# Kernel tuning notes

Hardware: AMD Instinct MI355X
Metric: run time of the kernel (lower is better)

The kernel has to match this reference:

```python
import jax, jax.numpy as jnp
import numpy as np

MARGIN = 0.3
EPS = 1e-12

def setup_inputs() -> dict:
    key = jax.random.key(0)
    k1, k2 = jax.random.split(key)
    B, D, NUM_IDS = 1024, 2048, 256
    features = jax.random.normal(k1, (B, D), dtype=jnp.float32)
    labels = jax.random.randint(k2, (B,), 0, NUM_IDS, dtype=jnp.int64)
    return {"features": features, "labels": labels}

def _pairwise_euclidean(features):
    # dist^2 = |x_i|^2 + |x_j|^2 - 2 x_i . x_j, clamped then sqrt (as in torch ref)
    sq = jnp.sum(features * features, axis=1)  # [B]
    d2 = sq[:, None] + sq[None, :] - 2.0 * (features @ features.T)
    return jnp.sqrt(jnp.maximum(d2, EPS))

def reference(features, labels):
    B = features.shape[0]
    dist = _pairwise_euclidean(features)  # [B, B]
    eq = labels[None, :] == labels[:, None]  # [B, B]; eq[i] == labels_equal row i
    eye = jnp.eye(B, dtype=bool)
    pos_mask = eq & ~eye
    neg_mask = ~eq
    neg_inf = jnp.float32(-jnp.inf)
    pos_inf = jnp.float32(jnp.inf)
    hardest_pos = jnp.max(jnp.where(pos_mask, dist, neg_inf), axis=1)  # [B]
    hardest_neg = jnp.min(jnp.where(neg_mask, dist, pos_inf), axis=1)  # [B]
    valid = jnp.any(pos_mask, axis=1) & jnp.any(neg_mask, axis=1)  # rows contributing a triplet
    per_row = jax.nn.relu(hardest_pos - hardest_neg + MARGIN)
    per_row = jnp.where(valid, per_row, 0.0)
    n_valid = jnp.sum(valid)
    loss = jnp.sum(per_row) / jnp.maximum(n_valid, 1).astype(per_row.dtype)
    num_active = jnp.sum(valid & (per_row > 0))
    return loss, num_active
```

## Files before the change

### kernel.cpp

```cpp
#include <hip/hip_runtime.h>
#include <math.h>

#define B_SZ 1024
#define D_SZ 2048
#define MARGIN 0.3f

typedef _Float16 f16x8 __attribute__((ext_vector_type(8)));
typedef float f32x16 __attribute__((ext_vector_type(16)));

union FragU { uint4 u; f16x8 v; };
union H4 { _Float16 h[4]; uint2 u; };



__global__ __launch_bounds__(256) void prep_kernel(const float* __restrict__ F,
                                                   _Float16* __restrict__ Fh,
                                                   float* __restrict__ sqpart,
                                                   int* __restrict__ hp,
                                                   int* __restrict__ hn,
                                                   int* __restrict__ flags) {
    __shared__ _Float16 slab[64][136];
    __shared__ float part[64];

    const int b = blockIdx.x;
    const int i = b >> 4;
    const int kseg = b & 15;
    const int t = threadIdx.x;
    const int lane = t & 63;
    const int w = t >> 6;

    const int idx = b * 256 + t;
    if (idx < 1024) {
        hp[idx] = 0;
        hn[idx] = 0x7F800000;
        flags[idx] = 0;
    }

#pragma unroll
    for (int q = 0; q < 8; ++q) {
        const int rl = q * 8 + (t >> 5);
        const int c4 = (t & 31) * 4;
        const float4 v = *(const float4*)(F + (size_t)(i * 64 + rl) * D_SZ +
                                          kseg * 128 + c4);
        float s = v.x * v.x + v.y * v.y + v.z * v.z + v.w * v.w;
#pragma unroll
        for (int mask = 1; mask < 32; mask <<= 1) s += __shfl_xor(s, mask);
        if ((t & 31) == 0) part[rl] = s;
        H4 p;
        p.h[0] = (_Float16)v.x; p.h[1] = (_Float16)v.y;
        p.h[2] = (_Float16)v.z; p.h[3] = (_Float16)v.w;
        *(uint2*)&slab[rl][c4] = p.u;
    }
    __syncthreads();

    if (t < 64) sqpart[kseg * 1024 + i * 64 + t] = part[t];

#pragma unroll
    for (int q2 = 0; q2 < 4; ++q2) {
        const int u = w * 4 + q2;
        const int kb = u >> 1;
        const int rg = u & 1;
        const uint4 d = *(const uint4*)&slab[rg * 32 + (lane & 31)]
                                          [kb * 16 + (lane >> 5) * 8];
        const size_t g = (size_t)((i * 128 + kseg * 8 + kb) * 2 + rg);
        *(uint4*)((char*)Fh + g * 1024 + (size_t)lane * 16) = d;
    }
}


__global__ __launch_bounds__(256) void dist_f16_kernel(
    const _Float16* __restrict__ Fh, const int* __restrict__ labels,
    const float* __restrict__ sqpart, int* __restrict__ hp,
    int* __restrict__ hn, int* __restrict__ flags) {
    __shared__ __align__(16) char comb[65536];
    __shared__ int labR[64], labC[64];
    __shared__ float sqR[64], sqC[64];

    const int t = threadIdx.x;
    const int lane = t & 63;
    const int w = t >> 6;

    const int tileId = (blockIdx.x & 7) * 32 + (blockIdx.x >> 3);
    const int bi = tileId >> 4;
    const int bj = tileId & 15;
    const int rowBase = bi * 64, colBase = bj * 64;

    if (t < 128) {
        const int e = t & 63;
        const int side = t >> 6;
        const int row = (side ? colBase : rowBase) + e;
        float s = 0.f;
#pragma unroll
        for (int p = 0; p < 16; ++p) s += sqpart[p * 1024 + row];
        if (side) { sqC[e] = s; labC[e] = labels[row]; }
        else      { sqR[e] = s; labR[e] = labels[row]; }
    }
    __syncthreads();

    const char* __restrict__ FhB = (const char*)Fh;

    f32x16 acc[2][2];
#pragma unroll
    for (int a = 0; a < 2; ++a)
#pragma unroll
        for (int c = 0; c < 2; ++c)
#pragma unroll
            for (int e = 0; e < 16; ++e) acc[a][c][e] = 0.f;

    uint4 A[3][4], Bv[3][4];

#define LOADAB(s, buf)                                                          \
    {                                                                           \
        const int kb16 = w * 32 + (s) * 2;                                      \
        _Pragma("unroll")                                                       \
        for (int kl = 0; kl < 2; ++kl)                                          \
            _Pragma("unroll")                                                   \
            for (int rg = 0; rg < 2; ++rg) {                                    \
                A[buf][kl * 2 + rg] = *(const uint4*)(FhB +                     \
                    (size_t)(((bi * 128 + kb16 + kl) * 2 + rg)) * 1024 +        \
                    (size_t)lane * 16);                                         \
                Bv[buf][kl * 2 + rg] = *(const uint4*)(FhB +                    \
                    (size_t)(((bj * 128 + kb16 + kl) * 2 + rg)) * 1024 +        \
                    (size_t)lane * 16);                                         \
            }                                                                   \
    }

#define MFMA8(buf)                                                              \
    {                                                                           \
        _Pragma("unroll")                                                       \
        for (int kl = 0; kl < 2; ++kl) {                                        \
            FragU a0, a1, v0, v1;                                               \
            a0.u = A[buf][kl * 2 + 0];                                          \
            a1.u = A[buf][kl * 2 + 1];                                          \
            v0.u = Bv[buf][kl * 2 + 0];                                         \
            v1.u = Bv[buf][kl * 2 + 1];                                         \
            acc[0][0] = __builtin_amdgcn_mfma_f32_32x32x16_f16(a0.v, v0.v, acc[0][0], 0, 0, 0); \
            acc[0][1] = __builtin_amdgcn_mfma_f32_32x32x16_f16(a0.v, v1.v, acc[0][1], 0, 0, 0); \
            acc[1][0] = __builtin_amdgcn_mfma_f32_32x32x16_f16(a1.v, v0.v, acc[1][0], 0, 0, 0); \
            acc[1][1] = __builtin_amdgcn_mfma_f32_32x32x16_f16(a1.v, v1.v, acc[1][1], 0, 0, 0); \
        }                                                                       \
    }

    LOADAB(0, 0);
    LOADAB(1, 1);
    LOADAB(2, 2);
#pragma unroll
    for (int s = 0; s < 16; ++s) {
        const int c = s % 3;
        MFMA8(c);
        if (s + 3 < 16) LOADAB(s + 3, c);
    }

#pragma unroll
    for (int fr = 0; fr < 2; ++fr)
#pragma unroll
        for (int fc = 0; fc < 2; ++fc)
#pragma unroll
            for (int g = 0; g < 4; ++g) {
                float4 v;
                v.x = acc[fr][fc][g * 4 + 0];
                v.y = acc[fr][fc][g * 4 + 1];
                v.z = acc[fr][fc][g * 4 + 2];
                v.w = acc[fr][fc][g * 4 + 3];
                *(float4*)(comb + ((size_t)((w * 16 + (fr * 2 + fc) * 4 + g) * 64 + lane)) * 16) = v;
            }
    __syncthreads();

    const int fr = w >> 1, fc = w & 1;
    float cS[16];
#pragma unroll
    for (int e = 0; e < 16; ++e) cS[e] = 0.f;
#pragma unroll
    for (int wp = 0; wp < 4; ++wp)
#pragma unroll
        for (int g = 0; g < 4; ++g) {
            float4 v = *(const float4*)(comb + ((size_t)((wp * 16 + w * 4 + g) * 64 + lane)) * 16);
            cS[g * 4 + 0] += v.x;
            cS[g * 4 + 1] += v.y;
            cS[g * 4 + 2] += v.z;
            cS[g * 4 + 3] += v.w;
        }

    const float BIG = 1e38f;
    const int h = lane >> 5;
    const int colL = fc * 32 + (lane & 31);
    const int j = colBase + colL;
    const int lj = labC[colL];
    const float sqj = sqC[colL];
#pragma unroll
    for (int k = 0; k < 16; ++k) {
        const int rowL = fr * 32 + (k & 3) + 8 * (k >> 2) + 4 * h;
        const int i = rowBase + rowL;
        const float d2 = sqR[rowL] + sqj - 2.f * cS[k];
        const float d = sqrtf(fmaxf(d2, 1e-12f));
        const bool eq = (labR[rowL] == lj);
        const bool isPos = eq && (i != j);
        float pv = isPos ? d : -BIG;
        float nv = eq ? BIG : d;
        int pf = (isPos ? 1 : 0) | (eq ? 0 : 2);
#pragma unroll
        for (int mask = 1; mask < 32; mask <<= 1) {
            pv = fmaxf(pv, __shfl_xor(pv, mask));
            nv = fminf(nv, __shfl_xor(nv, mask));
            pf |= __shfl_xor(pf, mask);
        }
        if ((lane & 31) == 0) {
            if (pf & 1) atomicMax(&hp[i], __float_as_int(pv));
            if (pf & 2) atomicMin(&hn[i], __float_as_int(nv));
            if (pf) atomicOr(&flags[i], pf);
        }
    }
#undef LOADAB
#undef MFMA8
}


__global__ __launch_bounds__(1024) void final_kernel(const int* __restrict__ hp,
                                                     const int* __restrict__ hn,
                                                     const int* __restrict__ flags,
                                                     float* __restrict__ out) {
    __shared__ float ssum[16];
    __shared__ int svalid[16], sact[16];
    const int t = threadIdx.x;
    const float hpv = __int_as_float(hp[t]);
    const float hnv = __int_as_float(hn[t]);
    const int f = flags[t];
    const bool valid = (f == 3);
    float pr = fmaxf(hpv - hnv + MARGIN, 0.f);
    if (!valid) pr = 0.f;
    int act = (valid && pr > 0.f) ? 1 : 0;
    int vld = valid ? 1 : 0;
    float s = pr;
    for (int off = 32; off; off >>= 1) {
        s += __shfl_down(s, off);
        act += __shfl_down(act, off);
        vld += __shfl_down(vld, off);
    }
    if ((t & 63) == 0) {
        ssum[t >> 6] = s;
        svalid[t >> 6] = vld;
        sact[t >> 6] = act;
    }
    __syncthreads();
    if (t == 0) {
        float tot = 0.f;
        int nv = 0, na = 0;
#pragma unroll
        for (int i = 0; i < 16; ++i) {
            tot += ssum[i];
            nv += svalid[i];
            na += sact[i];
        }
        out[0] = tot / (float)(nv > 1 ? nv : 1);
        out[1] = (float)na;
    }
}


#define BM 64
#define BN 64
#define BK 32

__global__ __launch_bounds__(256) void sq_kernel(const float* __restrict__ F,
                                                 float* __restrict__ sq) {
    int row = blockIdx.x;
    const float4* r4 = (const float4*)(F + (size_t)row * D_SZ);
    int t = threadIdx.x;
    float s = 0.f;
#pragma unroll
    for (int q = 0; q < 2; ++q) {
        float4 v = r4[t + q * 256];
        s += v.x * v.x + v.y * v.y + v.z * v.z + v.w * v.w;
    }
    for (int off = 32; off; off >>= 1) s += __shfl_down(s, off);
    __shared__ float wsum[4];
    if ((t & 63) == 0) wsum[t >> 6] = s;
    __syncthreads();
    if (t == 0) sq[row] = wsum[0] + wsum[1] + wsum[2] + wsum[3];
}

__global__ __launch_bounds__(256) void init_kernel(int* __restrict__ hp,
                                                   int* __restrict__ hn,
                                                   int* __restrict__ flags) {
    int i = blockIdx.x * 256 + threadIdx.x;
    hp[i] = 0;
    hn[i] = 0x7F800000;
    flags[i] = 0;
}

__global__ __launch_bounds__(256) void dist_f32_kernel(
    const float* __restrict__ F, const int* __restrict__ labels,
    const float* __restrict__ sq, int* __restrict__ hp, int* __restrict__ hn,
    int* __restrict__ flags) {
    __shared__ float As[BK][BM];
    __shared__ float Bs[BK][BN];
    __shared__ int labR[BM], labC[BN];
    __shared__ float sqR[BM], sqC[BN];

    const int rowBase = blockIdx.y * BM;
    const int colBase = blockIdx.x * BN;
    const int t = threadIdx.x;
    const int tx = t & 15;
    const int ty = t >> 4;

    if (t < 64) {
        labR[t] = labels[rowBase + t];
        sqR[t] = sq[rowBase + t];
    } else if (t < 128) {
        int u = t - 64;
        labC[u] = labels[colBase + u];
        sqC[u] = sq[colBase + u];
    }

    float acc[4][4] = {{0.f}};
    const int m = t & 63;
    const int q = t >> 6;
    const float* aRow = F + (size_t)(rowBase + m) * D_SZ + q * 8;
    const float* bRow = F + (size_t)(colBase + m) * D_SZ + q * 8;

    for (int k0 = 0; k0 < D_SZ; k0 += BK) {
        float4 a0 = *(const float4*)(aRow + k0);
        float4 a1 = *(const float4*)(aRow + k0 + 4);
        float4 b0 = *(const float4*)(bRow + k0);
        float4 b1 = *(const float4*)(bRow + k0 + 4);
        __syncthreads();
        int kb = q * 8;
        As[kb + 0][m] = a0.x; As[kb + 1][m] = a0.y;
        As[kb + 2][m] = a0.z; As[kb + 3][m] = a0.w;
        As[kb + 4][m] = a1.x; As[kb + 5][m] = a1.y;
        As[kb + 6][m] = a1.z; As[kb + 7][m] = a1.w;
        Bs[kb + 0][m] = b0.x; Bs[kb + 1][m] = b0.y;
        Bs[kb + 2][m] = b0.z; Bs[kb + 3][m] = b0.w;
        Bs[kb + 4][m] = b1.x; Bs[kb + 5][m] = b1.y;
        Bs[kb + 6][m] = b1.z; Bs[kb + 7][m] = b1.w;
        __syncthreads();
#pragma unroll
        for (int kk = 0; kk < BK; ++kk) {
            float4 a = *(const float4*)&As[kk][ty * 4];
            float4 b = *(const float4*)&Bs[kk][tx * 4];
            acc[0][0] += a.x * b.x; acc[0][1] += a.x * b.y;
            acc[0][2] += a.x * b.z; acc[0][3] += a.x * b.w;
            acc[1][0] += a.y * b.x; acc[1][1] += a.y * b.y;
            acc[1][2] += a.y * b.z; acc[1][3] += a.y * b.w;
            acc[2][0] += a.z * b.x; acc[2][1] += a.z * b.y;
            acc[2][2] += a.z * b.z; acc[2][3] += a.z * b.w;
            acc[3][0] += a.w * b.x; acc[3][1] += a.w * b.y;
            acc[3][2] += a.w * b.z; acc[3][3] += a.w * b.w;
        }
    }

    float mp[4], mn[4];
    int pf[4];
#pragma unroll
    for (int rr = 0; rr < 4; ++rr) {
        const int i = rowBase + ty * 4 + rr;
        const int li = labR[ty * 4 + rr];
        const float si = sqR[ty * 4 + rr];
        mp[rr] = -3.4e38f;
        mn[rr] = 3.4e38f;
        pf[rr] = 0;
#pragma unroll
        for (int c = 0; c < 4; ++c) {
            const int j = colBase + tx * 4 + c;
            const float d2 = si + sqC[tx * 4 + c] - 2.f * acc[rr][c];
            const float dist = sqrtf(fmaxf(d2, 1e-12f));
            const bool eq = (li == labC[tx * 4 + c]);
            if (eq && (i != j)) {
                mp[rr] = fmaxf(mp[rr], dist);
                pf[rr] |= 1;
            }
            if (!eq) {
                mn[rr] = fminf(mn[rr], dist);
                pf[rr] |= 2;
            }
        }
    }
#pragma unroll
    for (int mask = 1; mask < 16; mask <<= 1)
#pragma unroll
        for (int rr = 0; rr < 4; ++rr) {
            mp[rr] = fmaxf(mp[rr], __shfl_xor(mp[rr], mask));
            mn[rr] = fminf(mn[rr], __shfl_xor(mn[rr], mask));
            pf[rr] |= __shfl_xor(pf[rr], mask);
        }
    if (tx == 0) {
#pragma unroll
        for (int rr = 0; rr < 4; ++rr) {
            const int i = rowBase + ty * 4 + rr;
            if (pf[rr] & 1) atomicMax(&hp[i], __float_as_int(mp[rr]));
            if (pf[rr] & 2) atomicMin(&hn[i], __float_as_int(mn[rr]));
            if (pf[rr]) atomicOr(&flags[i], pf[rr]);
        }
    }
}


extern "C" void kernel_launch(void* const* d_in, const int* in_sizes, int n_in,
                              void* d_out, int out_size, void* d_ws, size_t ws_size,
                              hipStream_t stream) {
    const float* F = (const float*)d_in[0];
    const int* labels = (const int*)d_in[1];
    float* out = (float*)d_out;
    char* ws = (char*)d_ws;

    const size_t FH = (size_t)B_SZ * D_SZ * 2;
    const size_t SQP = 16 * 1024 * sizeof(float);
    const size_t need = FH + SQP + 12 * 1024;

    if (ws_size >= need) {
        _Float16* Fh = (_Float16*)ws;
        float* sqpart = (float*)(ws + FH);
        char* tail = ws + FH + SQP;
        int* hp = (int*)tail;
        int* hn = (int*)(tail + 4096);
        int* flags = (int*)(tail + 8192);

        prep_kernel<<<256, 256, 0, stream>>>(F, Fh, sqpart, hp, hn, flags);
        dist_f16_kernel<<<256, 256, 0, stream>>>(Fh, labels, sqpart, hp, hn, flags);
        final_kernel<<<1, 1024, 0, stream>>>(hp, hn, flags, out);
    } else {
        float* sq = (float*)ws;
        int* hp = (int*)(ws + 4096);
        int* hn = (int*)(ws + 8192);
        int* flags = (int*)(ws + 12288);

        sq_kernel<<<B_SZ, 256, 0, stream>>>(F, sq);
        init_kernel<<<B_SZ / 256, 256, 0, stream>>>(hp, hn, flags);
        dim3 grid(B_SZ / BN, B_SZ / BM);
        dist_f32_kernel<<<grid, 256, 0, stream>>>(F, labels, sq, hp, hn, flags);
        final_kernel<<<1, 1024, 0, stream>>>(hp, hn, flags, out);
    }
}
```

Before: 37.63 us.

## Split K across eight waves per block with two-stage cross-wave reduction

The distance tile kernel now launches 512 threads per block, giving each of eight waves half as many K steps. Partial accumulators are combined in two stages: the upper four waves add into the lower four through LDS, then the lower four exchange sub-tile fragments for the final sum. The prefetch pipeline now keeps four buffers, and the tile-to-XCD mapping is changed so each XCD covers a contiguous 4x8 block of tiles, meant to improve L2 reuse. The goal is more latency hiding per CU, paid for with an extra barrier, more LDS traffic and possible register pressure under the 512,2 launch bound.

```diff
diff --git a/kernel.cpp b/kernel.cpp
--- a/kernel.cpp
+++ b/kernel.cpp
@@ -68,7 +68,7 @@
 }
 
 
-__global__ __launch_bounds__(256) void dist_f16_kernel(
+__global__ __launch_bounds__(512, 2) void dist_f16_kernel(
     const _Float16* __restrict__ Fh, const int* __restrict__ labels,
     const float* __restrict__ sqpart, int* __restrict__ hp,
     int* __restrict__ hn, int* __restrict__ flags) {
@@ -80,9 +80,10 @@
     const int lane = t & 63;
     const int w = t >> 6;
 
-    const int tileId = (blockIdx.x & 7) * 32 + (blockIdx.x >> 3);
-    const int bi = tileId >> 4;
-    const int bj = tileId & 15;
+    const int xcd = blockIdx.x & 7;
+    const int cidx = blockIdx.x >> 3;
+    const int bi = (xcd >> 1) * 4 + (cidx >> 3);
+    const int bj = (xcd & 1) * 8 + (cidx & 7);
     const int rowBase = bi * 64, colBase = bj * 64;
 
     if (t < 128) {
@@ -107,11 +108,11 @@
 #pragma unroll
             for (int e = 0; e < 16; ++e) acc[a][c][e] = 0.f;
 
-    uint4 A[3][4], Bv[3][4];
+    uint4 A[4][4], Bv[4][4];
 
 #define LOADAB(s, buf)                                                          \
     {                                                                           \
-        const int kb16 = w * 32 + (s) * 2;                                      \
+        const int kb16 = w * 16 + (s) * 2;                                      \
         _Pragma("unroll")                                                       \
         for (int kl = 0; kl < 2; ++kl)                                          \
             _Pragma("unroll")                                                   \
@@ -145,16 +146,52 @@
     LOADAB(1, 1);
     LOADAB(2, 2);
 #pragma unroll
-    for (int s = 0; s < 16; ++s) {
-        const int c = s % 3;
-        MFMA8(c);
-        if (s + 3 < 16) LOADAB(s + 3, c);
-    }
-
-#pragma unroll
-    for (int fr = 0; fr < 2; ++fr)
-#pragma unroll
-        for (int fc = 0; fc < 2; ++fc)
+    for (int s = 0; s < 8; ++s) {
+        if (s + 3 < 8) LOADAB(s + 3, (s + 3) & 3);
+        MFMA8(s & 3);
+    }
+#undef LOADAB
+#undef MFMA8
+
+    if (w >= 4) {
+        char* r = comb + (w - 4) * 16384;
+#pragma unroll
+        for (int fr = 0; fr < 2; ++fr)
+#pragma unroll
+            for (int fc = 0; fc < 2; ++fc)
+#pragma unroll
+                for (int g = 0; g < 4; ++g) {
+                    float4 v;
+                    v.x = acc[fr][fc][g * 4 + 0];
+                    v.y = acc[fr][fc][g * 4 + 1];
+                    v.z = acc[fr][fc][g * 4 + 2];
+                    v.w = acc[fr][fc][g * 4 + 3];
+                    *(float4*)(r + (size_t)(((fr * 2 + fc) * 4 + g) * 64 + lane) * 16) = v;
+                }
+    }
+    __syncthreads();
+    if (w < 4) {
+        const char* r = comb + w * 16384;
+#pragma unroll
+        for (int fr = 0; fr < 2; ++fr)
+#pragma unroll
+            for (int fc = 0; fc < 2; ++fc)
+#pragma unroll
+                for (int g = 0; g < 4; ++g) {
+                    float4 v = *(const float4*)(r + (size_t)(((fr * 2 + fc) * 4 + g) * 64 + lane) * 16);
+                    acc[fr][fc][g * 4 + 0] += v.x;
+                    acc[fr][fc][g * 4 + 1] += v.y;
+                    acc[fr][fc][g * 4 + 2] += v.z;
+                    acc[fr][fc][g * 4 + 3] += v.w;
+                }
+    }
+    __syncthreads();
+    if (w < 4) {
+#pragma unroll
+        for (int f = 0; f < 4; ++f) {
+            if (f == w) continue;
+            char* r = comb + (size_t)(f * 4 + w) * 4096;
+            const int fr = f >> 1, fc = f & 1;
 #pragma unroll
             for (int g = 0; g < 4; ++g) {
                 float4 v;
@@ -162,56 +199,60 @@
                 v.y = acc[fr][fc][g * 4 + 1];
                 v.z = acc[fr][fc][g * 4 + 2];
                 v.w = acc[fr][fc][g * 4 + 3];
-                *(float4*)(comb + ((size_t)((w * 16 + (fr * 2 + fc) * 4 + g) * 64 + lane)) * 16) = v;
-            }
-    __syncthreads();
-
-    const int fr = w >> 1, fc = w & 1;
-    float cS[16];
-#pragma unroll
-    for (int e = 0; e < 16; ++e) cS[e] = 0.f;
-#pragma unroll
-    for (int wp = 0; wp < 4; ++wp)
-#pragma unroll
-        for (int g = 0; g < 4; ++g) {
-            float4 v = *(const float4*)(comb + ((size_t)((wp * 16 + w * 4 + g) * 64 + lane)) * 16);
-            cS[g * 4 + 0] += v.x;
-            cS[g * 4 + 1] += v.y;
-            cS[g * 4 + 2] += v.z;
-            cS[g * 4 + 3] += v.w;
-        }
-
-    const float BIG = 1e38f;
-    const int h = lane >> 5;
-    const int colL = fc * 32 + (lane & 31);
-    const int j = colBase + colL;
-    const int lj = labC[colL];
-    const float sqj = sqC[colL];
-#pragma unroll
-    for (int k = 0; k < 16; ++k) {
-        const int rowL = fr * 32 + (k & 3) + 8 * (k >> 2) + 4 * h;
-        const int i = rowBase + rowL;
-        const float d2 = sqR[rowL] + sqj - 2.f * cS[k];
-        const float d = sqrtf(fmaxf(d2, 1e-12f));
-        const bool eq = (labR[rowL] == lj);
-        const bool isPos = eq && (i != j);
-        float pv = isPos ? d : -BIG;
-        float nv = eq ? BIG : d;
-        int pf = (isPos ? 1 : 0) | (eq ? 0 : 2);
-#pragma unroll
-        for (int mask = 1; mask < 32; mask <<= 1) {
-            pv = fmaxf(pv, __shfl_xor(pv, mask));
-            nv = fminf(nv, __shfl_xor(nv, mask));
-            pf |= __shfl_xor(pf, mask);
-        }
-        if ((lane & 31) == 0) {
-            if (pf & 1) atomicMax(&hp[i], __float_as_int(pv));
-            if (pf & 2) atomicMin(&hn[i], __float_as_int(nv));
-            if (pf) atomicOr(&flags[i], pf);
-        }
-    }
-#undef LOADAB
-#undef MFMA8
+                *(float4*)(r + (size_t)(g * 64 + lane) * 16) = v;
+            }
+        }
+    }
+    __syncthreads();
+    if (w < 4) {
+        const int fr = w >> 1, fc = w & 1;
+        float cS[16];
+#pragma unroll
+        for (int e = 0; e < 16; ++e) cS[e] = acc[fr][fc][e];
+#pragma unroll
+        for (int u = 0; u < 4; ++u) {
+            if (u == w) continue;
+            const char* r = comb + (size_t)(w * 4 + u) * 4096;
+#pragma unroll
+            for (int g = 0; g < 4; ++g) {
+                float4 v = *(const float4*)(r + (size_t)(g * 64 + lane) * 16);
+                cS[g * 4 + 0] += v.x;
+                cS[g * 4 + 1] += v.y;
+                cS[g * 4 + 2] += v.z;
+                cS[g * 4 + 3] += v.w;
+            }
+        }
+
+        const float BIG = 1e38f;
+        const int h = lane >> 5;
+        const int colL = fc * 32 + (lane & 31);
+        const int j = colBase + colL;
+        const int lj = labC[colL];
+        const float sqj = sqC[colL];
+#pragma unroll
+        for (int k = 0; k < 16; ++k) {
+            const int rowL = fr * 32 + (k & 3) + 8 * (k >> 2) + 4 * h;
+            const int i = rowBase + rowL;
+            const float d2 = sqR[rowL] + sqj - 2.f * cS[k];
+            const float d = sqrtf(fmaxf(d2, 1e-12f));
+            const bool eq = (labR[rowL] == lj);
+            const bool isPos = eq && (i != j);
+            float pv = isPos ? d : -BIG;
+            float nv = eq ? BIG : d;
+            int pf = (isPos ? 1 : 0) | (eq ? 0 : 2);
+#pragma unroll
+            for (int mask = 1; mask < 32; mask <<= 1) {
+                pv = fmaxf(pv, __shfl_xor(pv, mask));
+                nv = fminf(nv, __shfl_xor(nv, mask));
+                pf |= __shfl_xor(pf, mask);
+            }
+            if ((lane & 31) == 0) {
+                if (pf & 1) atomicMax(&hp[i], __float_as_int(pv));
+                if (pf & 2) atomicMin(&hn[i], __float_as_int(nv));
+                if (pf) atomicOr(&flags[i], pf);
+            }
+        }
+    }
 }
 
 
@@ -416,7 +457,7 @@
         int* flags = (int*)(tail + 8192);
 
         prep_kernel<<<256, 256, 0, stream>>>(F, Fh, sqpart, hp, hn, flags);
-        dist_f16_kernel<<<256, 256, 0, stream>>>(Fh, labels, sqpart, hp, hn, flags);
+        dist_f16_kernel<<<256, 512, 0, stream>>>(Fh, labels, sqpart, hp, hn, flags);
         final_kernel<<<1, 1024, 0, stream>>>(hp, hn, flags, out);
     } else {
         float* sq = (float*)ws;
```

New measurement: 42.60 us. +13.2%, slower.

## Stage GEMM operands through LDS via direct global-to-LDS async loads

Applied to the files above, without the earlier changes.

Replaces register-buffered global loads in the distance GEMM with global_load_lds transfers into a per-wave triple-buffered LDS stage, using explicit vmcnt waits to overlap loads with MFMA. Operands are then read back from LDS for the MFMAs. The aim is to free VGPRs and make prefetch more asynchronous. In exchange it adds an LDS round trip, grows shared memory to 96KB (limiting occupancy), and depends on hand-tuned vmcnt counts being correct.

```diff
diff --git a/kernel.cpp b/kernel.cpp
--- a/kernel.cpp
+++ b/kernel.cpp
@@ -10,6 +10,9 @@
 
 union FragU { uint4 u; f16x8 v; };
 union H4 { _Float16 h[4]; uint2 u; };
+
+#define AS1 __attribute__((address_space(1)))
+#define AS3 __attribute__((address_space(3)))
 
 
 
@@ -68,11 +71,13 @@
 }
 
 
+#define WAVE_STAGE (3 * 8192)
+
 __global__ __launch_bounds__(256) void dist_f16_kernel(
     const _Float16* __restrict__ Fh, const int* __restrict__ labels,
     const float* __restrict__ sqpart, int* __restrict__ hp,
     int* __restrict__ hn, int* __restrict__ flags) {
-    __shared__ __align__(16) char comb[65536];
+    __shared__ __align__(16) char stage[4 * WAVE_STAGE];
     __shared__ int labR[64], labC[64];
     __shared__ float sqR[64], sqC[64];
 
@@ -96,8 +101,11 @@
         else      { sqR[e] = s; labR[e] = labels[row]; }
     }
     __syncthreads();
+    asm volatile("s_waitcnt vmcnt(0)" ::: "memory");
 
     const char* __restrict__ FhB = (const char*)Fh;
+    char* wbase = stage + w * WAVE_STAGE;
+    const char* rbase = wbase + lane * 16;
 
     f32x16 acc[2][2];
 #pragma unroll
@@ -107,50 +115,61 @@
 #pragma unroll
             for (int e = 0; e < 16; ++e) acc[a][c][e] = 0.f;
 
-    uint4 A[3][4], Bv[3][4];
-
-#define LOADAB(s, buf)                                                          \
-    {                                                                           \
-        const int kb16 = w * 32 + (s) * 2;                                      \
-        _Pragma("unroll")                                                       \
-        for (int kl = 0; kl < 2; ++kl)                                          \
-            _Pragma("unroll")                                                   \
-            for (int rg = 0; rg < 2; ++rg) {                                    \
-                A[buf][kl * 2 + rg] = *(const uint4*)(FhB +                     \
-                    (size_t)(((bi * 128 + kb16 + kl) * 2 + rg)) * 1024 +        \
-                    (size_t)lane * 16);                                         \
-                Bv[buf][kl * 2 + rg] = *(const uint4*)(FhB +                    \
-                    (size_t)(((bj * 128 + kb16 + kl) * 2 + rg)) * 1024 +        \
-                    (size_t)lane * 16);                                         \
-            }                                                                   \
-    }
-
-#define MFMA8(buf)                                                              \
-    {                                                                           \
-        _Pragma("unroll")                                                       \
-        for (int kl = 0; kl < 2; ++kl) {                                        \
-            FragU a0, a1, v0, v1;                                               \
-            a0.u = A[buf][kl * 2 + 0];                                          \
-            a1.u = A[buf][kl * 2 + 1];                                          \
-            v0.u = Bv[buf][kl * 2 + 0];                                         \
-            v1.u = Bv[buf][kl * 2 + 1];                                         \
-            acc[0][0] = __builtin_amdgcn_mfma_f32_32x32x16_f16(a0.v, v0.v, acc[0][0], 0, 0, 0); \
-            acc[0][1] = __builtin_amdgcn_mfma_f32_32x32x16_f16(a0.v, v1.v, acc[0][1], 0, 0, 0); \
-            acc[1][0] = __builtin_amdgcn_mfma_f32_32x32x16_f16(a1.v, v0.v, acc[1][0], 0, 0, 0); \
-            acc[1][1] = __builtin_amdgcn_mfma_f32_32x32x16_f16(a1.v, v1.v, acc[1][1], 0, 0, 0); \
-        }                                                                       \
-    }
-
-    LOADAB(0, 0);
-    LOADAB(1, 1);
-    LOADAB(2, 2);
-#pragma unroll
-    for (int s = 0; s < 16; ++s) {
-        const int c = s % 3;
-        MFMA8(c);
-        if (s + 3 < 16) LOADAB(s + 3, c);
-    }
-
+    auto ISSUE = [&](int s, int b) {
+        const int kb16 = w * 32 + s * 2;
+        const size_t aOff = (size_t)((bi * 128 + kb16) * 2) * 1024 + (size_t)lane * 16;
+        const size_t bOff = (size_t)((bj * 128 + kb16) * 2) * 1024 + (size_t)lane * 16;
+        char* dA = wbase + b * 8192;
+#pragma unroll
+        for (int c = 0; c < 4; ++c)
+            __builtin_amdgcn_global_load_lds(
+                (const AS1 void*)(FhB + aOff + c * 1024),
+                (AS3 void*)(dA + c * 1024), 16, 0, 0);
+#pragma unroll
+        for (int c = 0; c < 4; ++c)
+            __builtin_amdgcn_global_load_lds(
+                (const AS1 void*)(FhB + bOff + c * 1024),
+                (AS3 void*)(dA + 4096 + c * 1024), 16, 0, 0);
+    };
+    auto COMPUTE = [&](int b) {
+        const char* rb = rbase + b * 8192;
+#pragma unroll
+        for (int kl = 0; kl < 2; ++kl) {
+            FragU a0, a1, v0, v1;
+            a0.u = *(const uint4*)(rb + (kl * 2 + 0) * 1024);
+            a1.u = *(const uint4*)(rb + (kl * 2 + 1) * 1024);
+            v0.u = *(const uint4*)(rb + 4096 + (kl * 2 + 0) * 1024);
+            v1.u = *(const uint4*)(rb + 4096 + (kl * 2 + 1) * 1024);
+            acc[0][0] = __builtin_amdgcn_mfma_f32_32x32x16_f16(a0.v, v0.v, acc[0][0], 0, 0, 0);
+            acc[0][1] = __builtin_amdgcn_mfma_f32_32x32x16_f16(a0.v, v1.v, acc[0][1], 0, 0, 0);
+            acc[1][0] = __builtin_amdgcn_mfma_f32_32x32x16_f16(a1.v, v0.v, acc[1][0], 0, 0, 0);
+            acc[1][1] = __builtin_amdgcn_mfma_f32_32x32x16_f16(a1.v, v1.v, acc[1][1], 0, 0, 0);
+        }
+    };
+
+#define WAIT16 asm volatile("s_waitcnt vmcnt(16)" ::: "memory"); __builtin_amdgcn_sched_barrier(0)
+#define WAIT8  asm volatile("s_waitcnt vmcnt(8)"  ::: "memory"); __builtin_amdgcn_sched_barrier(0)
+#define WAIT0  asm volatile("s_waitcnt vmcnt(0)"  ::: "memory"); __builtin_amdgcn_sched_barrier(0)
+
+    ISSUE(0, 0);
+    ISSUE(1, 1);
+    for (int s3 = 0; s3 < 12; s3 += 3) {
+        ISSUE(s3 + 2, 2); WAIT16; COMPUTE(0);
+        ISSUE(s3 + 3, 0); WAIT16; COMPUTE(1);
+        ISSUE(s3 + 4, 1); WAIT16; COMPUTE(2);
+    }
+    ISSUE(14, 2); WAIT16; COMPUTE(0);
+    ISSUE(15, 0); WAIT16; COMPUTE(1);
+    WAIT8;  COMPUTE(2);
+    WAIT0;  COMPUTE(0);
+
+#undef WAIT16
+#undef WAIT8
+#undef WAIT0
+
+    __syncthreads();
+
+    char* cb = stage;
 #pragma unroll
     for (int fr = 0; fr < 2; ++fr)
 #pragma unroll
@@ -162,7 +181,7 @@
                 v.y = acc[fr][fc][g * 4 + 1];
                 v.z = acc[fr][fc][g * 4 + 2];
                 v.w = acc[fr][fc][g * 4 + 3];
-                *(float4*)(comb + ((size_t)((w * 16 + (fr * 2 + fc) * 4 + g) * 64 + lane)) * 16) = v;
+                *(float4*)(cb + ((size_t)((w * 16 + (fr * 2 + fc) * 4 + g) * 64 + lane)) * 16) = v;
             }
     __syncthreads();
 
@@ -174,7 +193,7 @@
     for (int wp = 0; wp < 4; ++wp)
 #pragma unroll
         for (int g = 0; g < 4; ++g) {
-            float4 v = *(const float4*)(comb + ((size_t)((wp * 16 + w * 4 + g) * 64 + lane)) * 16);
+            float4 v = *(const float4*)(cb + ((size_t)((wp * 16 + w * 4 + g) * 64 + lane)) * 16);
             cS[g * 4 + 0] += v.x;
             cS[g * 4 + 1] += v.y;
             cS[g * 4 + 2] += v.z;
@@ -210,8 +229,6 @@
             if (pf) atomicOr(&flags[i], pf);
         }
     }
-#undef LOADAB
-#undef MFMA8
 }
 
 
```

Result: faster. 31.97 us (median of 2 runs) (-15.0%).

## Split K across eight waves with tree reduction in dist kernel

Applied to the files above, without the earlier changes.

Doubles the dist kernel's block to 512 threads so eight waves each handle one eighth of the K dimension, with a shallower two-deep register double-buffer instead of the three-deep prefetch. Partial accumulators are combined through a three-stage shared-memory tree reduction, and wave 0 alone then runs the distance/mask epilogue for the whole 64x64 tile. The aim is more latency hiding per CU from more waves and fewer registers per wave. The cost is extra barriers and a serialized epilogue on a single wave.

```diff
diff --git a/kernel.cpp b/kernel.cpp
--- a/kernel.cpp
+++ b/kernel.cpp
@@ -68,11 +68,11 @@
 }
 
 
-__global__ __launch_bounds__(256) void dist_f16_kernel(
+__global__ __launch_bounds__(512) void dist_f16_kernel(
     const _Float16* __restrict__ Fh, const int* __restrict__ labels,
     const float* __restrict__ sqpart, int* __restrict__ hp,
     int* __restrict__ hn, int* __restrict__ flags) {
-    __shared__ __align__(16) char comb[65536];
+    __shared__ __align__(16) char cb[65536];
     __shared__ int labR[64], labC[64];
     __shared__ float sqR[64], sqC[64];
 
@@ -98,6 +98,8 @@
     __syncthreads();
 
     const char* __restrict__ FhB = (const char*)Fh;
+    const char* pA0 = FhB + (size_t)((bi * 128 + w * 16) * 2) * 1024 + (size_t)lane * 16;
+    const char* pB0 = FhB + (size_t)((bj * 128 + w * 16) * 2) * 1024 + (size_t)lane * 16;
 
     f32x16 acc[2][2];
 #pragma unroll
@@ -107,111 +109,120 @@
 #pragma unroll
             for (int e = 0; e < 16; ++e) acc[a][c][e] = 0.f;
 
-    uint4 A[3][4], Bv[3][4];
-
-#define LOADAB(s, buf)                                                          \
-    {                                                                           \
-        const int kb16 = w * 32 + (s) * 2;                                      \
-        _Pragma("unroll")                                                       \
-        for (int kl = 0; kl < 2; ++kl)                                          \
-            _Pragma("unroll")                                                   \
-            for (int rg = 0; rg < 2; ++rg) {                                    \
-                A[buf][kl * 2 + rg] = *(const uint4*)(FhB +                     \
-                    (size_t)(((bi * 128 + kb16 + kl) * 2 + rg)) * 1024 +        \
-                    (size_t)lane * 16);                                         \
-                Bv[buf][kl * 2 + rg] = *(const uint4*)(FhB +                    \
-                    (size_t)(((bj * 128 + kb16 + kl) * 2 + rg)) * 1024 +        \
-                    (size_t)lane * 16);                                         \
-            }                                                                   \
-    }
-
-#define MFMA8(buf)                                                              \
-    {                                                                           \
-        _Pragma("unroll")                                                       \
-        for (int kl = 0; kl < 2; ++kl) {                                        \
-            FragU a0, a1, v0, v1;                                               \
-            a0.u = A[buf][kl * 2 + 0];                                          \
-            a1.u = A[buf][kl * 2 + 1];                                          \
-            v0.u = Bv[buf][kl * 2 + 0];                                         \
-            v1.u = Bv[buf][kl * 2 + 1];                                         \
-            acc[0][0] = __builtin_amdgcn_mfma_f32_32x32x16_f16(a0.v, v0.v, acc[0][0], 0, 0, 0); \
-            acc[0][1] = __builtin_amdgcn_mfma_f32_32x32x16_f16(a0.v, v1.v, acc[0][1], 0, 0, 0); \
-            acc[1][0] = __builtin_amdgcn_mfma_f32_32x32x16_f16(a1.v, v0.v, acc[1][0], 0, 0, 0); \
-            acc[1][1] = __builtin_amdgcn_mfma_f32_32x32x16_f16(a1.v, v1.v, acc[1][1], 0, 0, 0); \
-        }                                                                       \
-    }
-
-    LOADAB(0, 0);
-    LOADAB(1, 1);
-    LOADAB(2, 2);
-#pragma unroll
-    for (int s = 0; s < 16; ++s) {
-        const int c = s % 3;
-        MFMA8(c);
-        if (s + 3 < 16) LOADAB(s + 3, c);
-    }
-
-#pragma unroll
-    for (int fr = 0; fr < 2; ++fr)
-#pragma unroll
-        for (int fc = 0; fc < 2; ++fc)
-#pragma unroll
-            for (int g = 0; g < 4; ++g) {
-                float4 v;
-                v.x = acc[fr][fc][g * 4 + 0];
-                v.y = acc[fr][fc][g * 4 + 1];
-                v.z = acc[fr][fc][g * 4 + 2];
-                v.w = acc[fr][fc][g * 4 + 3];
-                *(float4*)(comb + ((size_t)((w * 16 + (fr * 2 + fc) * 4 + g) * 64 + lane)) * 16) = v;
+    auto LOADREG = [&](int s, uint4* r) {
+        const size_t off = (size_t)s * 2048;
+        r[0] = *(const uint4*)(pA0 + off);
+        r[1] = *(const uint4*)(pA0 + off + 1024);
+        r[2] = *(const uint4*)(pB0 + off);
+        r[3] = *(const uint4*)(pB0 + off + 1024);
+    };
+    auto MFMA4 = [&](const uint4* r) {
+        FragU a0, a1, b0, b1;
+        a0.u = r[0];
+        a1.u = r[1];
+        b0.u = r[2];
+        b1.u = r[3];
+        acc[0][0] = __builtin_amdgcn_mfma_f32_32x32x16_f16(a0.v, b0.v, acc[0][0], 0, 0, 0);
+        acc[0][1] = __builtin_amdgcn_mfma_f32_32x32x16_f16(a0.v, b1.v, acc[0][1], 0, 0, 0);
+        acc[1][0] = __builtin_amdgcn_mfma_f32_32x32x16_f16(a1.v, b0.v, acc[1][0], 0, 0, 0);
+        acc[1][1] = __builtin_amdgcn_mfma_f32_32x32x16_f16(a1.v, b1.v, acc[1][1], 0, 0, 0);
+    };
+
+    uint4 ra[4], rb[4];
+    LOADREG(0, ra);
+#pragma unroll
+    for (int s = 0; s < 16; s += 2) {
+        LOADREG(s + 1, rb);
+        MFMA4(ra);
+        if (s + 2 < 16) LOADREG(s + 2, ra);
+        MFMA4(rb);
+    }
+
+    auto WRITE_PART = [&](int r) {
+        char* base = cb + (size_t)r * 16384;
+#pragma unroll
+        for (int fr = 0; fr < 2; ++fr)
+#pragma unroll
+            for (int fc = 0; fc < 2; ++fc)
+#pragma unroll
+                for (int g = 0; g < 4; ++g) {
+                    float4 v;
+                    v.x = acc[fr][fc][g * 4 + 0];
+                    v.y = acc[fr][fc][g * 4 + 1];
+                    v.z = acc[fr][fc][g * 4 + 2];
+                    v.w = acc[fr][fc][g * 4 + 3];
+                    *(float4*)(base + (size_t)(((fr * 2 + fc) * 4 + g) * 64 + lane) * 16) = v;
+                }
+    };
+    auto ADD_PART = [&](int r) {
+        const char* base = cb + (size_t)r * 16384;
+#pragma unroll
+        for (int fr = 0; fr < 2; ++fr)
+#pragma unroll
+            for (int fc = 0; fc < 2; ++fc)
+#pragma unroll
+                for (int g = 0; g < 4; ++g) {
+                    float4 v = *(const float4*)(base +
+                        (size_t)(((fr * 2 + fc) * 4 + g) * 64 + lane) * 16);
+                    acc[fr][fc][g * 4 + 0] += v.x;
+                    acc[fr][fc][g * 4 + 1] += v.y;
+                    acc[fr][fc][g * 4 + 2] += v.z;
+                    acc[fr][fc][g * 4 + 3] += v.w;
+                }
+    };
+
+    __syncthreads();
+    if (w >= 4) WRITE_PART(w - 4);
+    __syncthreads();
+    if (w < 4) ADD_PART(w);
+    __syncthreads();
+    if (w >= 2 && w < 4) WRITE_PART(w - 2);
+    __syncthreads();
+    if (w < 2) ADD_PART(w);
+    __syncthreads();
+    if (w == 1) WRITE_PART(0);
+    __syncthreads();
+
+    if (w == 0) {
+        ADD_PART(0);
+
+        const float BIG = 1e38f;
+        const int h = lane >> 5;
+#pragma unroll
+        for (int fr = 0; fr < 2; ++fr)
+#pragma unroll
+            for (int k = 0; k < 16; ++k) {
+                const int rowL = fr * 32 + (k & 3) + 8 * (k >> 2) + 4 * h;
+                const int i = rowBase + rowL;
+                const int li = labR[rowL];
+                const float sqi = sqR[rowL];
+                float pv = -BIG, nv = BIG;
+                int pf = 0;
+#pragma unroll
+                for (int fc = 0; fc < 2; ++fc) {
+                    const int colL = fc * 32 + (lane & 31);
+                    const int j = colBase + colL;
+                    const float d2 = sqi + sqC[colL] - 2.f * acc[fr][fc][k];
+                    const float d = sqrtf(fmaxf(d2, 1e-12f));
+                    const bool eq = (li == labC[colL]);
+                    const bool isPos = eq && (i != j);
+                    pv = fmaxf(pv, isPos ? d : -BIG);
+                    nv = fminf(nv, eq ? BIG : d);
+                    pf |= (isPos ? 1 : 0) | (eq ? 0 : 2);
+                }
+#pragma unroll
+                for (int mask = 1; mask < 32; mask <<= 1) {
+                    pv = fmaxf(pv, __shfl_xor(pv, mask));
+                    nv = fminf(nv, __shfl_xor(nv, mask));
+                    pf |= __shfl_xor(pf, mask);
+                }
+                if ((lane & 31) == 0) {
+                    if (pf & 1) atomicMax(&hp[i], __float_as_int(pv));
+                    if (pf & 2) atomicMin(&hn[i], __float_as_int(nv));
+                    if (pf) atomicOr(&flags[i], pf);
+                }
             }
-    __syncthreads();
-
-    const int fr = w >> 1, fc = w & 1;
-    float cS[16];
-#pragma unroll
-    for (int e = 0; e < 16; ++e) cS[e] = 0.f;
-#pragma unroll
-    for (int wp = 0; wp < 4; ++wp)
-#pragma unroll
-        for (int g = 0; g < 4; ++g) {
-            float4 v = *(const float4*)(comb + ((size_t)((wp * 16 + w * 4 + g) * 64 + lane)) * 16);
-            cS[g * 4 + 0] += v.x;
-            cS[g * 4 + 1] += v.y;
-            cS[g * 4 + 2] += v.z;
-            cS[g * 4 + 3] += v.w;
-        }
-
-    const float BIG = 1e38f;
-    const int h = lane >> 5;
-    const int colL = fc * 32 + (lane & 31);
-    const int j = colBase + colL;
-    const int lj = labC[colL];
-    const float sqj = sqC[colL];
-#pragma unroll
-    for (int k = 0; k < 16; ++k) {
-        const int rowL = fr * 32 + (k & 3) + 8 * (k >> 2) + 4 * h;
-        const int i = rowBase + rowL;
-        const float d2 = sqR[rowL] + sqj - 2.f * cS[k];
-        const float d = sqrtf(fmaxf(d2, 1e-12f));
-        const bool eq = (labR[rowL] == lj);
-        const bool isPos = eq && (i != j);
-        float pv = isPos ? d : -BIG;
-        float nv = eq ? BIG : d;
-        int pf = (isPos ? 1 : 0) | (eq ? 0 : 2);
-#pragma unroll
-        for (int mask = 1; mask < 32; mask <<= 1) {
-            pv = fmaxf(pv, __shfl_xor(pv, mask));
-            nv = fminf(nv, __shfl_xor(nv, mask));
-            pf |= __shfl_xor(pf, mask);
-        }
-        if ((lane & 31) == 0) {
-            if (pf & 1) atomicMax(&hp[i], __float_as_int(pv));
-            if (pf & 2) atomicMin(&hn[i], __float_as_int(nv));
-            if (pf) atomicOr(&flags[i], pf);
-        }
-    }
-#undef LOADAB
-#undef MFMA8
+    }
 }
 
 
@@ -416,7 +427,7 @@
         int* flags = (int*)(tail + 8192);
 
         prep_kernel<<<256, 256, 0, stream>>>(F, Fh, sqpart, hp, hn, flags);
-        dist_f16_kernel<<<256, 256, 0, stream>>>(Fh, labels, sqpart, hp, hn, flags);
+        dist_f16_kernel<<<256, 512, 0, stream>>>(Fh, labels, sqpart, hp, hn, flags);
         final_kernel<<<1, 1024, 0, stream>>>(hp, hn, flags, out);
     } else {
         float* sq = (float*)ws;
```

Result: slower. 40.98 us (+8.9%).
